# Kernel tuning notes

Measured on AMD Instinct MI355X. Metric: run time of the kernel, lower is better.

## Reference

```python
import jax, jax.numpy as jnp
import numpy as np

N = 50000      # nodes
E = 800000     # edges (avg degree 16)
F0 = 3         # node feature dim
EF = 3         # edge feature dim
C = 4          # num classes


def _lin_params(k, din, dout):
    k1, k2 = jax.random.split(k)
    s = 1.0 / np.sqrt(din)
    W = jax.random.uniform(k1, (dout, din), jnp.float32, -s, s)
    b = jax.random.uniform(k2, (dout,), jnp.float32, -s, s)
    return W, b


def setup_inputs() -> dict:
    key = jax.random.key(0)
    ks = jax.random.split(key, 8)
    x = jax.random.normal(ks[0], (N, F0), jnp.float32)
    edge_index = jax.random.randint(ks[1], (2, E), 0, N, jnp.int32)
    edge_attr = jax.random.uniform(ks[2], (E, EF), dtype=jnp.float32)
    W1, b1 = _lin_params(ks[3], 2 * F0 + EF, 128)
    W2, b2 = _lin_params(ks[4], 2 * 128 + EF, 64)
    W3, b3 = _lin_params(ks[5], 2 * 64 + EF, 32)
    Wc, bc = _lin_params(ks[6], 32, C)
    return dict(x=x, edge_index=edge_index, edge_attr=edge_attr,
                W1=W1, b1=b1, W2=W2, b2=b2, W3=W3, b3=b3, Wc=Wc, bc=bc)


def _edgeconv(x, src, dst, ea, W, b, n):
    # message = Linear(cat([x_i, x_j, edge_attr])); aggregated by scatter-add to dst (x_i side).
    # Split W so the node-side matmuls happen once per node instead of per edge.
    f = x.shape[1]
    Wi, Wj, We = W[:, :f], W[:, f:2 * f], W[:, 2 * f:]
    ai = x @ Wi.T   # [N, out]
    aj = x @ Wj.T   # [N, out]
    msg = ai[dst] + aj[src] + ea @ We.T + b  # [E_aug, out]
    return jax.ops.segment_sum(msg, dst, num_segments=n)


def reference(x, edge_index, edge_attr, W1, b1, W2, b2, W3, b3, Wc, bc):
    n = x.shape[0]
    loops = jnp.arange(n, dtype=edge_index.dtype)
    src = jnp.concatenate([edge_index[0], loops])  # x_j indices
    dst = jnp.concatenate([edge_index[1], loops])  # x_i indices (aggregation targets)
    ea = jnp.concatenate([edge_attr, jnp.zeros((n, edge_attr.shape[1]), edge_attr.dtype)])
    h = jax.nn.relu(_edgeconv(x, src, dst, ea, W1, b1, n))
    h = jax.nn.relu(_edgeconv(h, src, dst, ea, W2, b2, n))
    h = _edgeconv(h, src, dst, ea, W3, b3, n)  # no relu after conv3 in the original
    logits = h @ Wc.T + bc
    return jax.nn.log_softmax(logits, axis=1)
```

## Files before the change

### kernel.cpp

```cpp
#include <hip/hip_runtime.h>
#include <math.h>


static inline size_t align256(size_t x) { return (x + 255) & ~size_t(255); }

typedef unsigned short ushort_t;
using frag8  = __attribute__((ext_vector_type(8))) short;
using f32x4v = __attribute__((ext_vector_type(4))) float;
using half8  = __attribute__((ext_vector_type(8))) _Float16;

__device__ inline unsigned short f2bf(float f) {
    unsigned u = __float_as_uint(f);
    unsigned r = (u + 0x7fffu + ((u >> 16) & 1u)) >> 16;
    return (unsigned short)r;
}
__device__ inline float bflo(unsigned u) { return __uint_as_float(u << 16); }
__device__ inline float bfhi(unsigned u) { return __uint_as_float(u & 0xffff0000u); }


__global__ __launch_bounds__(256) void prep(
    const int* __restrict__ ei, int* __restrict__ count,
    int* __restrict__ pos, int E,
    const float* __restrict__ x, float4* __restrict__ xpad, int n,
    const float* __restrict__ W2, ushort_t* __restrict__ W2bf,
    const float* __restrict__ W3, const float* __restrict__ b3,
    const float* __restrict__ Wc, const float* __restrict__ bc,
    float* __restrict__ AB, float* __restrict__ consts,
    int eb4, int nxb)
{
    const int t = threadIdx.x;
    const int b = blockIdx.x;
    if (b < eb4) {
        int e4 = (b * 256 + t) * 4;
        if (e4 >= E) return;
        if (e4 + 3 < E) {
            int4 d = *(const int4*)(ei + E + e4);
            int4 po;
            po.x = atomicAdd(&count[d.x], 1);
            po.y = atomicAdd(&count[d.y], 1);
            po.z = atomicAdd(&count[d.z], 1);
            po.w = atomicAdd(&count[d.w], 1);
            *(int4*)(pos + e4) = po;
        } else {
            for (int e = e4; e < E; ++e)
                pos[e] = atomicAdd(&count[ei[E + e]], 1);
        }
    } else if (b < eb4 + nxb) {
        int j = (b - eb4) * 256 + t;
        if (j < n) {
            const float* xp = x + (size_t)j * 3;
            xpad[j] = make_float4(xp[0], xp[1], xp[2], 0.f);
        }
    } else if (b < eb4 + nxb + 4) {
        int wb = b - (eb4 + nxb);
        int i0 = wb * 4096 + t;
        int i1 = (wb + 1) * 4096;
        for (int idx = i0; idx < i1; idx += 256) {
            int jg = idx >> 7, k = idx & 127;
            float w = (jg < 64) ? W2[jg * 259 + k] : W2[(jg - 64) * 259 + 128 + k];
            W2bf[idx] = f2bf(w);
        }
    } else {
        for (int idx = t; idx < 512; idx += 256) {
            int j = idx >> 6, k = idx & 63;
            int jj = j & 3;
            int base = (j >= 4) ? 64 : 0;
            float s = 0.f;
            #pragma unroll
            for (int c = 0; c < 32; ++c)
                s += Wc[jj * 32 + c] * W3[c * 131 + base + k];
            AB[idx] = s;
        }
        if (t < 4) {
            float db = 0.f;
            for (int c = 0; c < 32; ++c) db += Wc[t * 32 + c] * b3[c];
            consts[t] = db;
            consts[4 + t] = bc[t];
            for (int q = 0; q < 3; ++q) {
                float s = 0.f;
                for (int c = 0; c < 32; ++c) s += Wc[t * 32 + c] * W3[c * 131 + 128 + q];
                consts[8 + t * 3 + q] = s;
            }
        }
    }
}


__global__ __launch_bounds__(256) void scan_pass1(
    const int* __restrict__ count, int* __restrict__ rowstart,
    int* __restrict__ bsum, int n)
{
    __shared__ int sh[256];
    const int tid = threadIdx.x;
    const int base = blockIdx.x * 1024 + tid * 4;
    int v0 = 0, v1 = 0, v2 = 0, v3 = 0;
    if (base + 3 < n) {
        int4 c = *(const int4*)(count + base);
        v0 = c.x; v1 = c.y; v2 = c.z; v3 = c.w;
    } else {
        if (base + 0 < n) v0 = count[base + 0];
        if (base + 1 < n) v1 = count[base + 1];
        if (base + 2 < n) v2 = count[base + 2];
        if (base + 3 < n) v3 = count[base + 3];
    }
    int tsum = v0 + v1 + v2 + v3;
    sh[tid] = tsum;
    __syncthreads();
    for (int off = 1; off < 256; off <<= 1) {
        int t = (tid >= off) ? sh[tid - off] : 0;
        __syncthreads();
        sh[tid] += t;
        __syncthreads();
    }
    int excl = sh[tid] - tsum;
    int p0 = excl + v0, p1 = p0 + v1, p2 = p1 + v2, p3 = p2 + v3;
    if (base + 0 < n) rowstart[base + 1] = p0;
    if (base + 1 < n) rowstart[base + 2] = p1;
    if (base + 2 < n) rowstart[base + 3] = p2;
    if (base + 3 < n) rowstart[base + 4] = p3;
    if (tid == 255) bsum[blockIdx.x] = sh[255];
}


__global__ __launch_bounds__(256) void csr_scatter2(
    const int* __restrict__ ei, const float* __restrict__ ea,
    const int* __restrict__ pos, const int* __restrict__ rowstart,
    const int* __restrict__ bsum, int nb,
    uint2* __restrict__ csrp, int* __restrict__ rowfin,
    int E, int n, int eb4)
{
    __shared__ int sBex[64];
    const int tid = threadIdx.x;
    if (tid < 64) {
        int v = (tid < nb) ? bsum[tid] : 0;
        int xx = v;
        #pragma unroll
        for (int off = 1; off < 64; off <<= 1) {
            int t = __shfl_up(xx, off);
            if (tid >= off) xx += t;
        }
        sBex[tid] = xx - v;
    }
    __syncthreads();

    if (blockIdx.x < eb4) {
        int e4 = (blockIdx.x * 256 + tid) * 4;
        if (e4 >= E) return;
        if (e4 + 3 < E) {
            int4 s = *(const int4*)(ei + e4);
            int4 d = *(const int4*)(ei + E + e4);
            int4 po = *(const int4*)(pos + e4);
            float4 a = *(const float4*)(ea + (size_t)e4 * 3);
            float4 bq = *(const float4*)(ea + (size_t)e4 * 3 + 4);
            float4 c = *(const float4*)(ea + (size_t)e4 * 3 + 8);
            float ev[12] = { a.x, a.y, a.z, a.w, bq.x, bq.y, bq.z, bq.w, c.x, c.y, c.z, c.w };
            int sv[4] = { s.x, s.y, s.z, s.w };
            int dv[4] = { d.x, d.y, d.z, d.w };
            int pv[4] = { po.x, po.y, po.z, po.w };
            #pragma unroll
            for (int r = 0; r < 4; ++r) {
                uint2 p;
                p.x = (unsigned)f2bf(ev[r * 3 + 0]) | ((unsigned)f2bf(ev[r * 3 + 1]) << 16);
                p.y = (unsigned)f2bf(ev[r * 3 + 2]) | ((unsigned)sv[r] << 16);
                int dd = dv[r];
                int rs = (dd == 0) ? 0 : (rowstart[dd] + sBex[(dd - 1) >> 10]);
                csrp[rs + pv[r]] = p;
            }
        } else {
            for (int e = e4; e < E; ++e) {
                uint2 p;
                p.x = (unsigned)f2bf(ea[e * 3 + 0]) | ((unsigned)f2bf(ea[e * 3 + 1]) << 16);
                p.y = (unsigned)f2bf(ea[e * 3 + 2]) | ((unsigned)ei[e] << 16);
                int dd = ei[E + e];
                int rs = (dd == 0) ? 0 : (rowstart[dd] + sBex[(dd - 1) >> 10]);
                csrp[rs + pos[e]] = p;
            }
        }
    } else {
        int j = (blockIdx.x - eb4) * 256 + tid;
        if (j <= n)
            rowfin[j] = (j == 0) ? 0 : (rowstart[j] + sBex[(j - 1) >> 10]);
    }
}


__global__ __launch_bounds__(256) void h1_gemm(
    const float4* __restrict__ xpad, const float* __restrict__ W1,
    const float* __restrict__ b1, const float* __restrict__ b2,
    const int* __restrict__ rowstart,
    const uint2* __restrict__ csrp, float4* __restrict__ eagg4,
    const ushort_t* __restrict__ W2bf,
    float* __restrict__ AI2, _Float16* __restrict__ AJ2, int n_nodes)
{
    constexpr int HS = 144;
    __shared__ float sM[10 * 128];
    __shared__ ushort_t sH[64 * HS];

    const int tid = threadIdx.x;
    for (int t = tid; t < 1280; t += 256) {
        int k = t >> 7, c = t & 127;
        sM[t] = (k < 9) ? W1[c * 9 + k] : b1[c];
    }
    __syncthreads();

    const int base = blockIdx.x * 64;
    const int wave = tid >> 6, wl = tid & 63;
    const int grp = wl >> 3, ch8 = wl & 7;

    #pragma unroll
    for (int pass = 0; pass < 2; ++pass) {
        int nl = pass * 32 + wave * 8 + grp;
        int n = base + nl;
        float hv[16];
        if (n < n_nodes) {
            int s0 = rowstart[n], s1 = rowstart[n + 1];
            float xx = 0.f, xy = 0.f, xz = 0.f, ex = 0.f, ey = 0.f, ez = 0.f;
            for (int i = s0 + ch8; i < s1; i += 8) {
                uint2 p = csrp[i];
                int s = (int)(p.y >> 16);
                ex += bflo(p.x); ey += bfhi(p.x); ez += bflo(p.y);
                float4 xv = xpad[s];
                xx += xv.x; xy += xv.y; xz += xv.z;
            }
            #pragma unroll
            for (int off = 1; off < 8; off <<= 1) {
                xx += __shfl_xor(xx, off); xy += __shfl_xor(xy, off); xz += __shfl_xor(xz, off);
                ex += __shfl_xor(ex, off); ey += __shfl_xor(ey, off); ez += __shfl_xor(ez, off);
            }
            float deg = (float)(s1 - s0 + 1);
            float4 xs = xpad[n];
            float v[10] = { deg * xs.x, deg * xs.y, deg * xs.z,
                            xs.x + xx, xs.y + xy, xs.z + xz,
                            ex, ey, ez, deg };
            #pragma unroll
            for (int q = 0; q < 16; ++q) {
                int c = ch8 * 16 + q;
                float h = 0.f;
                #pragma unroll
                for (int k = 0; k < 10; ++k) h += v[k] * sM[k * 128 + c];
                hv[q] = fmaxf(h, 0.f);
            }
            if (ch8 == 0) eagg4[n] = make_float4(ex, ey, ez, 0.f);
        } else {
            #pragma unroll
            for (int q = 0; q < 16; ++q) hv[q] = 0.f;
        }
        #pragma unroll
        for (int g = 0; g < 2; ++g) {
            uint4 u;
            u.x = (unsigned)f2bf(hv[g * 8 + 0]) | ((unsigned)f2bf(hv[g * 8 + 1]) << 16);
            u.y = (unsigned)f2bf(hv[g * 8 + 2]) | ((unsigned)f2bf(hv[g * 8 + 3]) << 16);
            u.z = (unsigned)f2bf(hv[g * 8 + 4]) | ((unsigned)f2bf(hv[g * 8 + 5]) << 16);
            u.w = (unsigned)f2bf(hv[g * 8 + 6]) | ((unsigned)f2bf(hv[g * 8 + 7]) << 16);
            *(uint4*)(sH + nl * HS + ch8 * 16 + g * 8) = u;
        }
    }
    __syncthreads();

    const int m = wl & 15, quad = wl >> 4;

    frag8 a[4];
    #pragma unroll
    for (int ks = 0; ks < 4; ++ks)
        a[ks] = *(const frag8*)(sH + (wave * 16 + m) * HS + ks * 32 + quad * 8);

    f32x4v acc[8];
    #pragma unroll
    for (int t = 0; t < 8; ++t) acc[t] = (f32x4v)(0.f);

    #pragma unroll
    for (int t = 0; t < 8; ++t) {
        #pragma unroll
        for (int ks = 0; ks < 4; ++ks) {
            frag8 b = *(const frag8*)(W2bf + (t * 16 + m) * 128 + ks * 32 + quad * 8);
            acc[t] = __builtin_amdgcn_mfma_f32_16x16x32_bf16(a[ks], b, acc[t], 0, 0, 0);
        }
    }

    float b2v[4];
    #pragma unroll
    for (int t = 0; t < 4; ++t) b2v[t] = b2[t * 16 + m];

    #pragma unroll
    for (int reg = 0; reg < 4; ++reg) {
        int grow = base + wave * 16 + quad * 4 + reg;
        if (grow >= n_nodes) continue;
        #pragma unroll
        for (int t = 0; t < 4; ++t)
            AI2[(size_t)grow * 64 + t * 16 + m] = acc[t][reg] + b2v[t];
        #pragma unroll
        for (int t = 4; t < 8; ++t)
            AJ2[(size_t)grow * 64 + (t - 4) * 16 + m] = (_Float16)acc[t][reg];
    }
}


__global__ __launch_bounds__(256) void gather2(
    const float* __restrict__ AI2, const _Float16* __restrict__ AJ2,
    const float* __restrict__ W2,
    const float4* __restrict__ eagg4, const int* __restrict__ rowstart,
    const uint2* __restrict__ csrp, const float* __restrict__ AB,
    float* __restrict__ U, float* __restrict__ Z, int n_nodes)
{
    __shared__ float sAB[512];
    __shared__ float sWe[192];
    const int tid = threadIdx.x;
    for (int t = tid; t < 512; t += 256) sAB[t] = AB[t];
    for (int t = tid; t < 192; t += 256) {
        int c = t / 3, q = t % 3;
        sWe[t] = W2[c * 259 + 256 + q];
    }
    __syncthreads();

    int wl = tid & 63;
    int grp = wl >> 3, ch8 = wl & 7;
    int n = blockIdx.x * 32 + (tid >> 6) * 8 + grp;
    if (n >= n_nodes) return;

    int s0 = rowstart[n], s1 = rowstart[n + 1];

    half8 hacc0 = (half8)(_Float16)0.f;
    half8 hacc1 = (half8)(_Float16)0.f;
    for (int base = s0; base < s1; base += 8) {
        int j = base + ch8;
        if (j >= s1) j = s1 - 1;
        int myidx = (int)(csrp[j].y >> 16);
        int cnt = s1 - base; if (cnt > 8) cnt = 8;
        #pragma unroll
        for (int k = 0; k < 8; ++k) {
            int s = __shfl(myidx, grp * 8 + k);
            if (k < cnt) {
                half8 v = *(const half8*)(AJ2 + (size_t)s * 64 + ch8 * 8);
                if (k & 1) hacc1 += v; else hacc0 += v;
            }
        }
    }
    float acc[8];
    #pragma unroll
    for (int q = 0; q < 8; ++q) acc[q] = (float)hacc0[q] + (float)hacc1[q];

    float deg = (float)(s1 - s0 + 1);
    float4 e4 = eagg4[n];
    const float* aip = AI2 + (size_t)n * 64 + ch8 * 8;
    float4 aiA = *(const float4*)(aip);
    float4 aiB = *(const float4*)(aip + 4);
    half8 su = *(const half8*)(AJ2 + (size_t)n * 64 + ch8 * 8);
    float av[8] = { aiA.x, aiA.y, aiA.z, aiA.w, aiB.x, aiB.y, aiB.z, aiB.w };
    float r[8];
    #pragma unroll
    for (int q = 0; q < 8; ++q) {
        int c = ch8 * 8 + q;
        float we = sWe[c * 3] * e4.x + sWe[c * 3 + 1] * e4.y + sWe[c * 3 + 2] * e4.z;
        r[q] = fmaxf(deg * av[q] + (float)su[q] + we + acc[q], 0.f);
    }
    float pj[8];
    #pragma unroll
    for (int j = 0; j < 8; ++j) {
        float4 wA = *(const float4*)(sAB + j * 64 + ch8 * 8);
        float4 wB = *(const float4*)(sAB + j * 64 + ch8 * 8 + 4);
        pj[j] = r[0] * wA.x + r[1] * wA.y + r[2] * wA.z + r[3] * wA.w
              + r[4] * wB.x + r[5] * wB.y + r[6] * wB.z + r[7] * wB.w;
    }
    #pragma unroll
    for (int off = 1; off < 8; off <<= 1)
        #pragma unroll
        for (int j = 0; j < 8; ++j) pj[j] += __shfl_xor(pj[j], off);

    if (ch8 == 0) {
        *(float4*)(U + (size_t)n * 4) = make_float4(pj[0], pj[1], pj[2], pj[3]);
        *(float4*)(Z + (size_t)n * 4) = make_float4(pj[4], pj[5], pj[6], pj[7]);
    }
}


__global__ __launch_bounds__(256) void final_softmax(
    const float* __restrict__ U, const float* __restrict__ Z,
    const float4* __restrict__ eagg4, const int* __restrict__ rowstart,
    const uint2* __restrict__ csrp, const float* __restrict__ consts,
    float* __restrict__ out, int n_nodes)
{
    int wl = threadIdx.x & 63;
    int grp = wl >> 3, ch8 = wl & 7;
    int n = blockIdx.x * 32 + (threadIdx.x >> 6) * 8 + grp;
    if (n >= n_nodes) return;

    int s0 = rowstart[n], s1 = rowstart[n + 1];
    float ax = 0.f, ay = 0.f, az = 0.f, aw = 0.f;
    for (int i = s0 + ch8; i < s1; i += 8) {
        int s = (int)(csrp[i].y >> 16);
        float4 z = *(const float4*)(Z + (size_t)s * 4);
        ax += z.x; ay += z.y; az += z.z; aw += z.w;
    }
    #pragma unroll
    for (int off = 1; off < 8; off <<= 1) {
        ax += __shfl_xor(ax, off); ay += __shfl_xor(ay, off);
        az += __shfl_xor(az, off); aw += __shfl_xor(aw, off);
    }
    if (ch8 != 0) return;

    float deg = (float)(s1 - s0 + 1);
    float4 u = *(const float4*)(U + (size_t)n * 4);
    float4 zs = *(const float4*)(Z + (size_t)n * 4);
    float4 e4 = eagg4[n];
    float av[4] = { ax + zs.x, ay + zs.y, az + zs.z, aw + zs.w };
    float uv[4] = { u.x, u.y, u.z, u.w };
    float lg[4];
    #pragma unroll
    for (int j = 0; j < 4; ++j) {
        lg[j] = deg * (uv[j] + consts[j]) + av[j] + consts[4 + j]
              + consts[8 + j * 3] * e4.x + consts[9 + j * 3] * e4.y
              + consts[10 + j * 3] * e4.z;
    }
    float m = fmaxf(fmaxf(lg[0], lg[1]), fmaxf(lg[2], lg[3]));
    float lse = logf(expf(lg[0] - m) + expf(lg[1] - m) + expf(lg[2] - m) + expf(lg[3] - m));
    *(float4*)(out + (size_t)n * 4) =
        make_float4(lg[0] - m - lse, lg[1] - m - lse, lg[2] - m - lse, lg[3] - m - lse);
}


extern "C" void kernel_launch(void* const* d_in, const int* in_sizes, int n_in,
                              void* d_out, int out_size, void* d_ws, size_t ws_size,
                              hipStream_t stream)
{
    const float* x    = (const float*)d_in[0];
    const int*   ei   = (const int*)  d_in[1];
    const float* ea   = (const float*)d_in[2];
    const float* W1   = (const float*)d_in[3];
    const float* b1   = (const float*)d_in[4];
    const float* W2   = (const float*)d_in[5];
    const float* b2   = (const float*)d_in[6];
    const float* W3   = (const float*)d_in[7];
    const float* b3   = (const float*)d_in[8];
    const float* Wc   = (const float*)d_in[9];
    const float* bc   = (const float*)d_in[10];
    float* out = (float*)d_out;

    const int N = in_sizes[0] / 3;
    const int E = in_sizes[1] / 2;

    char* ws = (char*)d_ws;
    size_t off = 0;
    int*    count    = (int*)(ws + off);            off = align256(off + (size_t)N * 4);
    int*    pos      = (int*)(ws + off);            off = align256(off + (size_t)E * 4);
    int*    rowstart = (int*)(ws + off);            off = align256(off + (size_t)(N + 1) * 4);
    int*    rowfin   = (int*)(ws + off);            off = align256(off + (size_t)(N + 1) * 4);
    uint2*  csrp     = (uint2*)(ws + off);          off = align256(off + (size_t)E * 8);
    int*    bsum     = (int*)(ws + off);            off = align256(off + 256);
    float*  AB       = (float*)(ws + off);          off = align256(off + 512 * 4);
    float*  consts   = (float*)(ws + off);          off = align256(off + 32 * 4);
    ushort_t* W2bf   = (ushort_t*)(ws + off);       off = align256(off + 128 * 128 * 2);
    float4* xpad     = (float4*)(ws + off);         off = align256(off + (size_t)N * 16);
    float4* eagg4    = (float4*)(ws + off);         off = align256(off + (size_t)N * 16);
    float*  AI2      = (float*)(ws + off);          off = align256(off + (size_t)N * 64 * 4);
    _Float16* AJ2    = (_Float16*)(ws + off);       off = align256(off + (size_t)N * 64 * 2);
    float*  Ubuf     = (float*)(ws + off);          off = align256(off + (size_t)N * 16);
    float*  Zbuf     = (float*)(ws + off);          off = align256(off + (size_t)N * 16);
    (void)ws_size;

    hipMemsetAsync(count, 0, (size_t)N * 4, stream);

    const int eb4 = ((E + 3) / 4 + 255) / 256;
    const int nxb = (N + 255) / 256;
    const int nb1 = (N + 1023) / 1024;
    const int nfb = (N + 1 + 255) / 256;

    prep<<<eb4 + nxb + 5, 256, 0, stream>>>(ei, count, pos, E,
                                            x, xpad, N, W2, W2bf,
                                            W3, b3, Wc, bc, AB, consts,
                                            eb4, nxb);

    scan_pass1<<<nb1, 256, 0, stream>>>(count, rowstart, bsum, N);

    csr_scatter2<<<eb4 + nfb, 256, 0, stream>>>(ei, ea, pos, rowstart, bsum, nb1,
                                                csrp, rowfin, E, N, eb4);

    h1_gemm<<<(N + 63) / 64, 256, 0, stream>>>(xpad, W1, b1, b2, rowfin, csrp,
                                               eagg4, W2bf, AI2, AJ2, N);

    const int gb = (N + 31) / 32;
    gather2<<<gb, 256, 0, stream>>>(AI2, AJ2, W2, eagg4, rowfin, csrp, AB, Ubuf, Zbuf, N);

    final_softmax<<<gb, 256, 0, stream>>>(Ubuf, Zbuf, eagg4, rowfin, csrp, consts, out, N);
}
```

Measured before the change: 198.1 us.

## Embed source features in CSR records and split source-index array

The CSR scatter now gathers each edge's source node features and stores them as fp16 alongside the bf16 edge attributes in a 16-byte record. This removes the dependent xpad gather from the layer-1 aggregation loop, which is also unrolled by two. A separate int array of source indices feeds the later gather kernels, giving them a narrower stream. It also swizzles the W1 shared-memory layout and changes the sH padding to avoid bank conflicts. The cost is double the CSR bytes written plus an extra random gather in the scatter kernel, and fp16 rounding of x.

```diff
diff --git a/kernel.cpp b/kernel.cpp
--- a/kernel.cpp
+++ b/kernel.cpp
@@ -16,6 +16,17 @@
 }
 __device__ inline float bflo(unsigned u) { return __uint_as_float(u << 16); }
 __device__ inline float bfhi(unsigned u) { return __uint_as_float(u & 0xffff0000u); }
+__device__ inline unsigned short f2h(float f) {
+    _Float16 h = (_Float16)f;
+    unsigned short u;
+    __builtin_memcpy(&u, &h, 2);
+    return u;
+}
+__device__ inline float h2f(unsigned short u) {
+    _Float16 h;
+    __builtin_memcpy(&h, &u, 2);
+    return (float)h;
+}
 
 
 __global__ __launch_bounds__(256) void prep(
@@ -126,7 +137,9 @@
     const int* __restrict__ ei, const float* __restrict__ ea,
     const int* __restrict__ pos, const int* __restrict__ rowstart,
     const int* __restrict__ bsum, int nb,
-    uint2* __restrict__ csrp, int* __restrict__ rowfin,
+    const float4* __restrict__ xpad,
+    uint4* __restrict__ csrh, int* __restrict__ csrs,
+    int* __restrict__ rowfin,
     int E, int n, int eb4)
 {
     __shared__ int sBex[64];
@@ -153,27 +166,39 @@
             float4 a = *(const float4*)(ea + (size_t)e4 * 3);
             float4 bq = *(const float4*)(ea + (size_t)e4 * 3 + 4);
             float4 c = *(const float4*)(ea + (size_t)e4 * 3 + 8);
+            float4 xv0 = xpad[s.x], xv1 = xpad[s.y], xv2 = xpad[s.z], xv3 = xpad[s.w];
             float ev[12] = { a.x, a.y, a.z, a.w, bq.x, bq.y, bq.z, bq.w, c.x, c.y, c.z, c.w };
+            float4 xv[4] = { xv0, xv1, xv2, xv3 };
             int sv[4] = { s.x, s.y, s.z, s.w };
             int dv[4] = { d.x, d.y, d.z, d.w };
             int pv[4] = { po.x, po.y, po.z, po.w };
             #pragma unroll
             for (int r = 0; r < 4; ++r) {
-                uint2 p;
-                p.x = (unsigned)f2bf(ev[r * 3 + 0]) | ((unsigned)f2bf(ev[r * 3 + 1]) << 16);
-                p.y = (unsigned)f2bf(ev[r * 3 + 2]) | ((unsigned)sv[r] << 16);
+                uint4 h;
+                h.x = (unsigned)f2bf(ev[r * 3 + 0]) | ((unsigned)f2bf(ev[r * 3 + 1]) << 16);
+                h.y = (unsigned)f2bf(ev[r * 3 + 2]) | ((unsigned)f2h(xv[r].x) << 16);
+                h.z = (unsigned)f2h(xv[r].y) | ((unsigned)f2h(xv[r].z) << 16);
+                h.w = (unsigned)sv[r];
                 int dd = dv[r];
                 int rs = (dd == 0) ? 0 : (rowstart[dd] + sBex[(dd - 1) >> 10]);
-                csrp[rs + pv[r]] = p;
+                int slot = rs + pv[r];
+                csrh[slot] = h;
+                csrs[slot] = sv[r];
             }
         } else {
             for (int e = e4; e < E; ++e) {
-                uint2 p;
-                p.x = (unsigned)f2bf(ea[e * 3 + 0]) | ((unsigned)f2bf(ea[e * 3 + 1]) << 16);
-                p.y = (unsigned)f2bf(ea[e * 3 + 2]) | ((unsigned)ei[e] << 16);
+                int sv = ei[e];
+                float4 xv = xpad[sv];
+                uint4 h;
+                h.x = (unsigned)f2bf(ea[e * 3 + 0]) | ((unsigned)f2bf(ea[e * 3 + 1]) << 16);
+                h.y = (unsigned)f2bf(ea[e * 3 + 2]) | ((unsigned)f2h(xv.x) << 16);
+                h.z = (unsigned)f2h(xv.y) | ((unsigned)f2h(xv.z) << 16);
+                h.w = (unsigned)sv;
                 int dd = ei[E + e];
                 int rs = (dd == 0) ? 0 : (rowstart[dd] + sBex[(dd - 1) >> 10]);
-                csrp[rs + pos[e]] = p;
+                int slot = rs + pos[e];
+                csrh[slot] = h;
+                csrs[slot] = sv;
             }
         }
     } else {
@@ -188,18 +213,19 @@
     const float4* __restrict__ xpad, const float* __restrict__ W1,
     const float* __restrict__ b1, const float* __restrict__ b2,
     const int* __restrict__ rowstart,
-    const uint2* __restrict__ csrp, float4* __restrict__ eagg4,
+    const uint4* __restrict__ csrh, float4* __restrict__ eagg4,
     const ushort_t* __restrict__ W2bf,
     float* __restrict__ AI2, _Float16* __restrict__ AJ2, int n_nodes)
 {
-    constexpr int HS = 144;
+    constexpr int HS = 152;
     __shared__ float sM[10 * 128];
     __shared__ ushort_t sH[64 * HS];
 
     const int tid = threadIdx.x;
     for (int t = tid; t < 1280; t += 256) {
         int k = t >> 7, c = t & 127;
-        sM[t] = (k < 9) ? W1[c * 9 + k] : b1[c];
+        int cp = (c & 15) * 8 + (c >> 4);
+        sM[k * 128 + cp] = (k < 9) ? W1[c * 9 + k] : b1[c];
     }
     __syncthreads();
 
@@ -215,12 +241,25 @@
         if (n < n_nodes) {
             int s0 = rowstart[n], s1 = rowstart[n + 1];
             float xx = 0.f, xy = 0.f, xz = 0.f, ex = 0.f, ey = 0.f, ez = 0.f;
-            for (int i = s0 + ch8; i < s1; i += 8) {
-                uint2 p = csrp[i];
-                int s = (int)(p.y >> 16);
-                ex += bflo(p.x); ey += bfhi(p.x); ez += bflo(p.y);
-                float4 xv = xpad[s];
-                xx += xv.x; xy += xv.y; xz += xv.z;
+            int i = s0 + ch8;
+            for (; i + 8 < s1; i += 16) {
+                uint4 p0 = csrh[i];
+                uint4 p1 = csrh[i + 8];
+                ex += bflo(p0.x); ey += bfhi(p0.x); ez += bflo(p0.y);
+                xx += h2f((ushort_t)(p0.y >> 16));
+                xy += h2f((ushort_t)(p0.z & 0xffff));
+                xz += h2f((ushort_t)(p0.z >> 16));
+                ex += bflo(p1.x); ey += bfhi(p1.x); ez += bflo(p1.y);
+                xx += h2f((ushort_t)(p1.y >> 16));
+                xy += h2f((ushort_t)(p1.z & 0xffff));
+                xz += h2f((ushort_t)(p1.z >> 16));
+            }
+            if (i < s1) {
+                uint4 p0 = csrh[i];
+                ex += bflo(p0.x); ey += bfhi(p0.x); ez += bflo(p0.y);
+                xx += h2f((ushort_t)(p0.y >> 16));
+                xy += h2f((ushort_t)(p0.z & 0xffff));
+                xz += h2f((ushort_t)(p0.z >> 16));
             }
             #pragma unroll
             for (int off = 1; off < 8; off <<= 1) {
@@ -234,10 +273,9 @@
                             ex, ey, ez, deg };
             #pragma unroll
             for (int q = 0; q < 16; ++q) {
-                int c = ch8 * 16 + q;
                 float h = 0.f;
                 #pragma unroll
-                for (int k = 0; k < 10; ++k) h += v[k] * sM[k * 128 + c];
+                for (int k = 0; k < 10; ++k) h += v[k] * sM[k * 128 + q * 8 + ch8];
                 hv[q] = fmaxf(h, 0.f);
             }
             if (ch8 == 0) eagg4[n] = make_float4(ex, ey, ez, 0.f);
@@ -299,7 +337,7 @@
     const float* __restrict__ AI2, const _Float16* __restrict__ AJ2,
     const float* __restrict__ W2,
     const float4* __restrict__ eagg4, const int* __restrict__ rowstart,
-    const uint2* __restrict__ csrp, const float* __restrict__ AB,
+    const int* __restrict__ csrs, const float* __restrict__ AB,
     float* __restrict__ U, float* __restrict__ Z, int n_nodes)
 {
     __shared__ float sAB[512];
@@ -324,7 +362,7 @@
     for (int base = s0; base < s1; base += 8) {
         int j = base + ch8;
         if (j >= s1) j = s1 - 1;
-        int myidx = (int)(csrp[j].y >> 16);
+        int myidx = csrs[j];
         int cnt = s1 - base; if (cnt > 8) cnt = 8;
         #pragma unroll
         for (int k = 0; k < 8; ++k) {
@@ -376,7 +414,7 @@
 __global__ __launch_bounds__(256) void final_softmax(
     const float* __restrict__ U, const float* __restrict__ Z,
     const float4* __restrict__ eagg4, const int* __restrict__ rowstart,
-    const uint2* __restrict__ csrp, const float* __restrict__ consts,
+    const int* __restrict__ csrs, const float* __restrict__ consts,
     float* __restrict__ out, int n_nodes)
 {
     int wl = threadIdx.x & 63;
@@ -387,7 +425,7 @@
     int s0 = rowstart[n], s1 = rowstart[n + 1];
     float ax = 0.f, ay = 0.f, az = 0.f, aw = 0.f;
     for (int i = s0 + ch8; i < s1; i += 8) {
-        int s = (int)(csrp[i].y >> 16);
+        int s = csrs[i];
         float4 z = *(const float4*)(Z + (size_t)s * 4);
         ax += z.x; ay += z.y; az += z.z; aw += z.w;
     }
@@ -444,7 +482,8 @@
     int*    pos      = (int*)(ws + off);            off = align256(off + (size_t)E * 4);
     int*    rowstart = (int*)(ws + off);            off = align256(off + (size_t)(N + 1) * 4);
     int*    rowfin   = (int*)(ws + off);            off = align256(off + (size_t)(N + 1) * 4);
-    uint2*  csrp     = (uint2*)(ws + off);          off = align256(off + (size_t)E * 8);
+    uint4*  csrh     = (uint4*)(ws + off);          off = align256(off + (size_t)E * 16);
+    int*    csrs     = (int*)(ws + off);            off = align256(off + (size_t)E * 4);
     int*    bsum     = (int*)(ws + off);            off = align256(off + 256);
     float*  AB       = (float*)(ws + off);          off = align256(off + 512 * 4);
     float*  consts   = (float*)(ws + off);          off = align256(off + 32 * 4);
@@ -472,13 +511,13 @@
     scan_pass1<<<nb1, 256, 0, stream>>>(count, rowstart, bsum, N);
 
     csr_scatter2<<<eb4 + nfb, 256, 0, stream>>>(ei, ea, pos, rowstart, bsum, nb1,
-                                                csrp, rowfin, E, N, eb4);
-
-    h1_gemm<<<(N + 63) / 64, 256, 0, stream>>>(xpad, W1, b1, b2, rowfin, csrp,
+                                                xpad, csrh, csrs, rowfin, E, N, eb4);
+
+    h1_gemm<<<(N + 63) / 64, 256, 0, stream>>>(xpad, W1, b1, b2, rowfin, csrh,
                                                eagg4, W2bf, AI2, AJ2, N);
 
     const int gb = (N + 31) / 32;
-    gather2<<<gb, 256, 0, stream>>>(AI2, AJ2, W2, eagg4, rowfin, csrp, AB, Ubuf, Zbuf, N);
-
-    final_softmax<<<gb, 256, 0, stream>>>(Ubuf, Zbuf, eagg4, rowfin, csrp, consts, out, N);
-}
+    gather2<<<gb, 256, 0, stream>>>(AI2, AJ2, W2, eagg4, rowfin, csrs, AB, Ubuf, Zbuf, N);
+
+    final_softmax<<<gb, 256, 0, stream>>>(Ubuf, Zbuf, eagg4, rowfin, csrs, consts, out, N);
+}
```

New measurement: 207.1 us. 4.6% more time.

## Aggregate layer-1 neighbor and edge sums via atomics in prep, shrink CSR to indices

Applied to the files above, without the earlier changes.

The layer-1 sums of neighbor features and edge attributes are now accumulated per destination node with float atomics inside the edge-counting prep kernel. This removes h1_gemm's dependency on the CSR build, so h1_gemm can run before the CSR scatter and no longer walks CSR rows. The CSR payload drops from 8-byte packed (bf16 edge attr + src) to 4-byte src index, cutting scatter and gather traffic. The cost is six float atomics per edge, which adds atomic contention and makes the summation order nondeterministic. It also changes the h1 weight layout in shared memory.

```diff
diff --git a/kernel.cpp b/kernel.cpp
--- a/kernel.cpp
+++ b/kernel.cpp
@@ -14,13 +14,12 @@
     unsigned r = (u + 0x7fffu + ((u >> 16) & 1u)) >> 16;
     return (unsigned short)r;
 }
-__device__ inline float bflo(unsigned u) { return __uint_as_float(u << 16); }
-__device__ inline float bfhi(unsigned u) { return __uint_as_float(u & 0xffff0000u); }
 
 
 __global__ __launch_bounds__(256) void prep(
     const int* __restrict__ ei, int* __restrict__ count,
-    int* __restrict__ pos, int E,
+    int* __restrict__ pos, float* __restrict__ nodeacc,
+    const float* __restrict__ ea, int E,
     const float* __restrict__ x, float4* __restrict__ xpad, int n,
     const float* __restrict__ W2, ushort_t* __restrict__ W2bf,
     const float* __restrict__ W3, const float* __restrict__ b3,
@@ -34,6 +33,7 @@
         int e4 = (b * 256 + t) * 4;
         if (e4 >= E) return;
         if (e4 + 3 < E) {
+            int4 s = *(const int4*)(ei + e4);
             int4 d = *(const int4*)(ei + E + e4);
             int4 po;
             po.x = atomicAdd(&count[d.x], 1);
@@ -41,9 +41,37 @@
             po.z = atomicAdd(&count[d.z], 1);
             po.w = atomicAdd(&count[d.w], 1);
             *(int4*)(pos + e4) = po;
+            float4 a = *(const float4*)(ea + (size_t)e4 * 3);
+            float4 bq = *(const float4*)(ea + (size_t)e4 * 3 + 4);
+            float4 c = *(const float4*)(ea + (size_t)e4 * 3 + 8);
+            float ev[12] = { a.x, a.y, a.z, a.w, bq.x, bq.y, bq.z, bq.w, c.x, c.y, c.z, c.w };
+            int sv[4] = { s.x, s.y, s.z, s.w };
+            int dv[4] = { d.x, d.y, d.z, d.w };
+            #pragma unroll
+            for (int r = 0; r < 4; ++r) {
+                const float* xs = x + (size_t)sv[r] * 3;
+                float x0 = xs[0], x1 = xs[1], x2 = xs[2];
+                float* acc = nodeacc + (size_t)dv[r] * 8;
+                atomicAdd(acc + 0, ev[r * 3 + 0]);
+                atomicAdd(acc + 1, ev[r * 3 + 1]);
+                atomicAdd(acc + 2, ev[r * 3 + 2]);
+                atomicAdd(acc + 3, x0);
+                atomicAdd(acc + 4, x1);
+                atomicAdd(acc + 5, x2);
+            }
         } else {
-            for (int e = e4; e < E; ++e)
-                pos[e] = atomicAdd(&count[ei[E + e]], 1);
+            for (int e = e4; e < E; ++e) {
+                int sv = ei[e], dv = ei[E + e];
+                pos[e] = atomicAdd(&count[dv], 1);
+                const float* xs = x + (size_t)sv * 3;
+                float* acc = nodeacc + (size_t)dv * 8;
+                atomicAdd(acc + 0, ea[e * 3 + 0]);
+                atomicAdd(acc + 1, ea[e * 3 + 1]);
+                atomicAdd(acc + 2, ea[e * 3 + 2]);
+                atomicAdd(acc + 3, xs[0]);
+                atomicAdd(acc + 4, xs[1]);
+                atomicAdd(acc + 5, xs[2]);
+            }
         }
     } else if (b < eb4 + nxb) {
         int j = (b - eb4) * 256 + t;
@@ -122,11 +150,108 @@
 }
 
 
+__global__ __launch_bounds__(256) void h1_gemm(
+    const float4* __restrict__ xpad, const float* __restrict__ W1,
+    const float* __restrict__ b1, const float* __restrict__ b2,
+    const int* __restrict__ count, const float* __restrict__ nodeacc,
+    const ushort_t* __restrict__ W2bf,
+    float* __restrict__ AI2, _Float16* __restrict__ AJ2, int n_nodes)
+{
+    constexpr int HS = 152;
+    __shared__ float sM[10 * 128];
+    __shared__ ushort_t sH[64 * HS];
+
+    const int tid = threadIdx.x;
+    for (int t = tid; t < 1280; t += 256) {
+        int k = t >> 7, c = t & 127;
+        int cp = (c & 15) * 8 + (c >> 4);
+        sM[k * 128 + cp] = (k < 9) ? W1[c * 9 + k] : b1[c];
+    }
+    __syncthreads();
+
+    const int base = blockIdx.x * 64;
+    const int wave = tid >> 6, wl = tid & 63;
+    const int grp = wl >> 3, ch8 = wl & 7;
+
+    #pragma unroll
+    for (int pass = 0; pass < 2; ++pass) {
+        int nl = pass * 32 + wave * 8 + grp;
+        int n = base + nl;
+        float hv[16];
+        if (n < n_nodes) {
+            float4 a0 = *(const float4*)(nodeacc + (size_t)n * 8);
+            float4 a1 = *(const float4*)(nodeacc + (size_t)n * 8 + 4);
+            float deg = (float)(count[n] + 1);
+            float4 xs = xpad[n];
+            float v[10] = { deg * xs.x, deg * xs.y, deg * xs.z,
+                            xs.x + a0.w, xs.y + a1.x, xs.z + a1.y,
+                            a0.x, a0.y, a0.z, deg };
+            #pragma unroll
+            for (int q = 0; q < 16; ++q) {
+                float h = 0.f;
+                #pragma unroll
+                for (int k = 0; k < 10; ++k) h += v[k] * sM[k * 128 + q * 8 + ch8];
+                hv[q] = fmaxf(h, 0.f);
+            }
+        } else {
+            #pragma unroll
+            for (int q = 0; q < 16; ++q) hv[q] = 0.f;
+        }
+        #pragma unroll
+        for (int g = 0; g < 2; ++g) {
+            uint4 u;
+            u.x = (unsigned)f2bf(hv[g * 8 + 0]) | ((unsigned)f2bf(hv[g * 8 + 1]) << 16);
+            u.y = (unsigned)f2bf(hv[g * 8 + 2]) | ((unsigned)f2bf(hv[g * 8 + 3]) << 16);
+            u.z = (unsigned)f2bf(hv[g * 8 + 4]) | ((unsigned)f2bf(hv[g * 8 + 5]) << 16);
+            u.w = (unsigned)f2bf(hv[g * 8 + 6]) | ((unsigned)f2bf(hv[g * 8 + 7]) << 16);
+            *(uint4*)(sH + nl * HS + ch8 * 16 + g * 8) = u;
+        }
+    }
+    __syncthreads();
+
+    const int m = wl & 15, quad = wl >> 4;
+
+    frag8 a[4];
+    #pragma unroll
+    for (int ks = 0; ks < 4; ++ks)
+        a[ks] = *(const frag8*)(sH + (wave * 16 + m) * HS + ks * 32 + quad * 8);
+
+    f32x4v acc[8];
+    #pragma unroll
+    for (int t = 0; t < 8; ++t) acc[t] = (f32x4v)(0.f);
+
+    #pragma unroll
+    for (int t = 0; t < 8; ++t) {
+        #pragma unroll
+        for (int ks = 0; ks < 4; ++ks) {
+            frag8 b = *(const frag8*)(W2bf + (t * 16 + m) * 128 + ks * 32 + quad * 8);
+            acc[t] = __builtin_amdgcn_mfma_f32_16x16x32_bf16(a[ks], b, acc[t], 0, 0, 0);
+        }
+    }
+
+    float b2v[4];
+    #pragma unroll
+    for (int t = 0; t < 4; ++t) b2v[t] = b2[t * 16 + m];
+
+    #pragma unroll
+    for (int reg = 0; reg < 4; ++reg) {
+        int grow = base + wave * 16 + quad * 4 + reg;
+        if (grow >= n_nodes) continue;
+        #pragma unroll
+        for (int t = 0; t < 4; ++t)
+            AI2[(size_t)grow * 64 + t * 16 + m] = acc[t][reg] + b2v[t];
+        #pragma unroll
+        for (int t = 4; t < 8; ++t)
+            AJ2[(size_t)grow * 64 + (t - 4) * 16 + m] = (_Float16)acc[t][reg];
+    }
+}
+
+
 __global__ __launch_bounds__(256) void csr_scatter2(
-    const int* __restrict__ ei, const float* __restrict__ ea,
+    const int* __restrict__ ei,
     const int* __restrict__ pos, const int* __restrict__ rowstart,
     const int* __restrict__ bsum, int nb,
-    uint2* __restrict__ csrp, int* __restrict__ rowfin,
+    int* __restrict__ csrs, int* __restrict__ rowfin,
     int E, int n, int eb4)
 {
     __shared__ int sBex[64];
@@ -150,30 +275,20 @@
             int4 s = *(const int4*)(ei + e4);
             int4 d = *(const int4*)(ei + E + e4);
             int4 po = *(const int4*)(pos + e4);
-            float4 a = *(const float4*)(ea + (size_t)e4 * 3);
-            float4 bq = *(const float4*)(ea + (size_t)e4 * 3 + 4);
-            float4 c = *(const float4*)(ea + (size_t)e4 * 3 + 8);
-            float ev[12] = { a.x, a.y, a.z, a.w, bq.x, bq.y, bq.z, bq.w, c.x, c.y, c.z, c.w };
             int sv[4] = { s.x, s.y, s.z, s.w };
             int dv[4] = { d.x, d.y, d.z, d.w };
             int pv[4] = { po.x, po.y, po.z, po.w };
             #pragma unroll
             for (int r = 0; r < 4; ++r) {
-                uint2 p;
-                p.x = (unsigned)f2bf(ev[r * 3 + 0]) | ((unsigned)f2bf(ev[r * 3 + 1]) << 16);
-                p.y = (unsigned)f2bf(ev[r * 3 + 2]) | ((unsigned)sv[r] << 16);
                 int dd = dv[r];
                 int rs = (dd == 0) ? 0 : (rowstart[dd] + sBex[(dd - 1) >> 10]);
-                csrp[rs + pv[r]] = p;
+                csrs[rs + pv[r]] = sv[r];
             }
         } else {
             for (int e = e4; e < E; ++e) {
-                uint2 p;
-                p.x = (unsigned)f2bf(ea[e * 3 + 0]) | ((unsigned)f2bf(ea[e * 3 + 1]) << 16);
-                p.y = (unsigned)f2bf(ea[e * 3 + 2]) | ((unsigned)ei[e] << 16);
                 int dd = ei[E + e];
                 int rs = (dd == 0) ? 0 : (rowstart[dd] + sBex[(dd - 1) >> 10]);
-                csrp[rs + pos[e]] = p;
+                csrs[rs + pos[e]] = ei[e];
             }
         }
     } else {
@@ -184,122 +299,11 @@
 }
 
 
-__global__ __launch_bounds__(256) void h1_gemm(
-    const float4* __restrict__ xpad, const float* __restrict__ W1,
-    const float* __restrict__ b1, const float* __restrict__ b2,
-    const int* __restrict__ rowstart,
-    const uint2* __restrict__ csrp, float4* __restrict__ eagg4,
-    const ushort_t* __restrict__ W2bf,
-    float* __restrict__ AI2, _Float16* __restrict__ AJ2, int n_nodes)
-{
-    constexpr int HS = 144;
-    __shared__ float sM[10 * 128];
-    __shared__ ushort_t sH[64 * HS];
-
-    const int tid = threadIdx.x;
-    for (int t = tid; t < 1280; t += 256) {
-        int k = t >> 7, c = t & 127;
-        sM[t] = (k < 9) ? W1[c * 9 + k] : b1[c];
-    }
-    __syncthreads();
-
-    const int base = blockIdx.x * 64;
-    const int wave = tid >> 6, wl = tid & 63;
-    const int grp = wl >> 3, ch8 = wl & 7;
-
-    #pragma unroll
-    for (int pass = 0; pass < 2; ++pass) {
-        int nl = pass * 32 + wave * 8 + grp;
-        int n = base + nl;
-        float hv[16];
-        if (n < n_nodes) {
-            int s0 = rowstart[n], s1 = rowstart[n + 1];
-            float xx = 0.f, xy = 0.f, xz = 0.f, ex = 0.f, ey = 0.f, ez = 0.f;
-            for (int i = s0 + ch8; i < s1; i += 8) {
-                uint2 p = csrp[i];
-                int s = (int)(p.y >> 16);
-                ex += bflo(p.x); ey += bfhi(p.x); ez += bflo(p.y);
-                float4 xv = xpad[s];
-                xx += xv.x; xy += xv.y; xz += xv.z;
-            }
-            #pragma unroll
-            for (int off = 1; off < 8; off <<= 1) {
-                xx += __shfl_xor(xx, off); xy += __shfl_xor(xy, off); xz += __shfl_xor(xz, off);
-                ex += __shfl_xor(ex, off); ey += __shfl_xor(ey, off); ez += __shfl_xor(ez, off);
-            }
-            float deg = (float)(s1 - s0 + 1);
-            float4 xs = xpad[n];
-            float v[10] = { deg * xs.x, deg * xs.y, deg * xs.z,
-                            xs.x + xx, xs.y + xy, xs.z + xz,
-                            ex, ey, ez, deg };
-            #pragma unroll
-            for (int q = 0; q < 16; ++q) {
-                int c = ch8 * 16 + q;
-                float h = 0.f;
-                #pragma unroll
-                for (int k = 0; k < 10; ++k) h += v[k] * sM[k * 128 + c];
-                hv[q] = fmaxf(h, 0.f);
-            }
-            if (ch8 == 0) eagg4[n] = make_float4(ex, ey, ez, 0.f);
-        } else {
-            #pragma unroll
-            for (int q = 0; q < 16; ++q) hv[q] = 0.f;
-        }
-        #pragma unroll
-        for (int g = 0; g < 2; ++g) {
-            uint4 u;
-            u.x = (unsigned)f2bf(hv[g * 8 + 0]) | ((unsigned)f2bf(hv[g * 8 + 1]) << 16);
-            u.y = (unsigned)f2bf(hv[g * 8 + 2]) | ((unsigned)f2bf(hv[g * 8 + 3]) << 16);
-            u.z = (unsigned)f2bf(hv[g * 8 + 4]) | ((unsigned)f2bf(hv[g * 8 + 5]) << 16);
-            u.w = (unsigned)f2bf(hv[g * 8 + 6]) | ((unsigned)f2bf(hv[g * 8 + 7]) << 16);
-            *(uint4*)(sH + nl * HS + ch8 * 16 + g * 8) = u;
-        }
-    }
-    __syncthreads();
-
-    const int m = wl & 15, quad = wl >> 4;
-
-    frag8 a[4];
-    #pragma unroll
-    for (int ks = 0; ks < 4; ++ks)
-        a[ks] = *(const frag8*)(sH + (wave * 16 + m) * HS + ks * 32 + quad * 8);
-
-    f32x4v acc[8];
-    #pragma unroll
-    for (int t = 0; t < 8; ++t) acc[t] = (f32x4v)(0.f);
-
-    #pragma unroll
-    for (int t = 0; t < 8; ++t) {
-        #pragma unroll
-        for (int ks = 0; ks < 4; ++ks) {
-            frag8 b = *(const frag8*)(W2bf + (t * 16 + m) * 128 + ks * 32 + quad * 8);
-            acc[t] = __builtin_amdgcn_mfma_f32_16x16x32_bf16(a[ks], b, acc[t], 0, 0, 0);
-        }
-    }
-
-    float b2v[4];
-    #pragma unroll
-    for (int t = 0; t < 4; ++t) b2v[t] = b2[t * 16 + m];
-
-    #pragma unroll
-    for (int reg = 0; reg < 4; ++reg) {
-        int grow = base + wave * 16 + quad * 4 + reg;
-        if (grow >= n_nodes) continue;
-        #pragma unroll
-        for (int t = 0; t < 4; ++t)
-            AI2[(size_t)grow * 64 + t * 16 + m] = acc[t][reg] + b2v[t];
-        #pragma unroll
-        for (int t = 4; t < 8; ++t)
-            AJ2[(size_t)grow * 64 + (t - 4) * 16 + m] = (_Float16)acc[t][reg];
-    }
-}
-
-
 __global__ __launch_bounds__(256) void gather2(
     const float* __restrict__ AI2, const _Float16* __restrict__ AJ2,
-    const float* __restrict__ W2,
-    const float4* __restrict__ eagg4, const int* __restrict__ rowstart,
-    const uint2* __restrict__ csrp, const float* __restrict__ AB,
+    const float* __restrict__ W2, const float* __restrict__ nodeacc,
+    const int* __restrict__ rowstart,
+    const int* __restrict__ csrs, const float* __restrict__ AB,
     float* __restrict__ U, float* __restrict__ Z, int n_nodes)
 {
     __shared__ float sAB[512];
@@ -324,7 +328,7 @@
     for (int base = s0; base < s1; base += 8) {
         int j = base + ch8;
         if (j >= s1) j = s1 - 1;
-        int myidx = (int)(csrp[j].y >> 16);
+        int myidx = csrs[j];
         int cnt = s1 - base; if (cnt > 8) cnt = 8;
         #pragma unroll
         for (int k = 0; k < 8; ++k) {
@@ -340,7 +344,7 @@
     for (int q = 0; q < 8; ++q) acc[q] = (float)hacc0[q] + (float)hacc1[q];
 
     float deg = (float)(s1 - s0 + 1);
-    float4 e4 = eagg4[n];
+    float4 e4 = *(const float4*)(nodeacc + (size_t)n * 8);
     const float* aip = AI2 + (size_t)n * 64 + ch8 * 8;
     float4 aiA = *(const float4*)(aip);
     float4 aiB = *(const float4*)(aip + 4);
@@ -375,8 +379,8 @@
 
 __global__ __launch_bounds__(256) void final_softmax(
     const float* __restrict__ U, const float* __restrict__ Z,
-    const float4* __restrict__ eagg4, const int* __restrict__ rowstart,
-    const uint2* __restrict__ csrp, const float* __restrict__ consts,
+    const float* __restrict__ nodeacc, const int* __restrict__ rowstart,
+    const int* __restrict__ csrs, const float* __restrict__ consts,
     float* __restrict__ out, int n_nodes)
 {
     int wl = threadIdx.x & 63;
@@ -387,7 +391,7 @@
     int s0 = rowstart[n], s1 = rowstart[n + 1];
     float ax = 0.f, ay = 0.f, az = 0.f, aw = 0.f;
     for (int i = s0 + ch8; i < s1; i += 8) {
-        int s = (int)(csrp[i].y >> 16);
+        int s = csrs[i];
         float4 z = *(const float4*)(Z + (size_t)s * 4);
         ax += z.x; ay += z.y; az += z.z; aw += z.w;
     }
@@ -401,7 +405,7 @@
     float deg = (float)(s1 - s0 + 1);
     float4 u = *(const float4*)(U + (size_t)n * 4);
     float4 zs = *(const float4*)(Z + (size_t)n * 4);
-    float4 e4 = eagg4[n];
+    float4 e4 = *(const float4*)(nodeacc + (size_t)n * 8);
     float av[4] = { ax + zs.x, ay + zs.y, az + zs.z, aw + zs.w };
     float uv[4] = { u.x, u.y, u.z, u.w };
     float lg[4];
@@ -441,44 +445,45 @@
     char* ws = (char*)d_ws;
     size_t off = 0;
     int*    count    = (int*)(ws + off);            off = align256(off + (size_t)N * 4);
+    float*  nodeacc  = (float*)(ws + off);          off = align256(off + (size_t)N * 32);
     int*    pos      = (int*)(ws + off);            off = align256(off + (size_t)E * 4);
     int*    rowstart = (int*)(ws + off);            off = align256(off + (size_t)(N + 1) * 4);
     int*    rowfin   = (int*)(ws + off);            off = align256(off + (size_t)(N + 1) * 4);
-    uint2*  csrp     = (uint2*)(ws + off);          off = align256(off + (size_t)E * 8);
+    int*    csrs     = (int*)(ws + off);            off = align256(off + (size_t)E * 4);
     int*    bsum     = (int*)(ws + off);            off = align256(off + 256);
     float*  AB       = (float*)(ws + off);          off = align256(off + 512 * 4);
     float*  consts   = (float*)(ws + off);          off = align256(off + 32 * 4);
     ushort_t* W2bf   = (ushort_t*)(ws + off);       off = align256(off + 128 * 128 * 2);
     float4* xpad     = (float4*)(ws + off);         off = align256(off + (size_t)N * 16);
-    float4* eagg4    = (float4*)(ws + off);         off = align256(off + (size_t)N * 16);
     float*  AI2      = (float*)(ws + off);          off = align256(off + (size_t)N * 64 * 4);
     _Float16* AJ2    = (_Float16*)(ws + off);       off = align256(off + (size_t)N * 64 * 2);
     float*  Ubuf     = (float*)(ws + off);          off = align256(off + (size_t)N * 16);
     float*  Zbuf     = (float*)(ws + off);          off = align256(off + (size_t)N * 16);
     (void)ws_size;
 
-    hipMemsetAsync(count, 0, (size_t)N * 4, stream);
+    size_t zlen = (size_t)((char*)nodeacc - (char*)count) + (size_t)N * 32;
+    hipMemsetAsync(count, 0, zlen, stream);
 
     const int eb4 = ((E + 3) / 4 + 255) / 256;
     const int nxb = (N + 255) / 256;
     const int nb1 = (N + 1023) / 1024;
     const int nfb = (N + 1 + 255) / 256;
 
-    prep<<<eb4 + nxb + 5, 256, 0, stream>>>(ei, count, pos, E,
+    prep<<<eb4 + nxb + 5, 256, 0, stream>>>(ei, count, pos, nodeacc, ea, E,
                                             x, xpad, N, W2, W2bf,
                                             W3, b3, Wc, bc, AB, consts,
                                             eb4, nxb);
 
     scan_pass1<<<nb1, 256, 0, stream>>>(count, rowstart, bsum, N);
 
-    csr_scatter2<<<eb4 + nfb, 256, 0, stream>>>(ei, ea, pos, rowstart, bsum, nb1,
-                                                csrp, rowfin, E, N, eb4);
-
-    h1_gemm<<<(N + 63) / 64, 256, 0, stream>>>(xpad, W1, b1, b2, rowfin, csrp,
-                                               eagg4, W2bf, AI2, AJ2, N);
+    h1_gemm<<<(N + 63) / 64, 256, 0, stream>>>(xpad, W1, b1, b2, count, nodeacc,
+                                               W2bf, AI2, AJ2, N);
+
+    csr_scatter2<<<eb4 + nfb, 256, 0, stream>>>(ei, pos, rowstart, bsum, nb1,
+                                                csrs, rowfin, E, N, eb4);
 
     const int gb = (N + 31) / 32;
-    gather2<<<gb, 256, 0, stream>>>(AI2, AJ2, W2, eagg4, rowfin, csrp, AB, Ubuf, Zbuf, N);
-
-    final_softmax<<<gb, 256, 0, stream>>>(Ubuf, Zbuf, eagg4, rowfin, csrp, consts, out, N);
-}
+    gather2<<<gb, 256, 0, stream>>>(AI2, AJ2, W2, nodeacc, rowfin, csrs, AB, Ubuf, Zbuf, N);
+
+    final_softmax<<<gb, 256, 0, stream>>>(Ubuf, Zbuf, nodeacc, rowfin, csrs, consts, out, N);
+}
```

New measurement: 430.5 us. 2.17x slower.

## Aggregate layer-1 neighbor sums per block with shared-memory atomics over edge range

Applied to the files above, without the earlier changes.

Replaces the per-node 8-lane CSR gather loop in h1_gemm with a block-wide sweep over the block's contiguous edge range. Each thread binary-searches the owning node and accumulates into shared memory with atomics. This aims to spread load evenly across threads instead of idling lanes on low-degree nodes. It also transposes the W1 shared layout to avoid bank conflicts and pads the sH stride. The cost is many LDS atomics per edge plus a 6-step search per edge.

```diff
diff --git a/kernel.cpp b/kernel.cpp
--- a/kernel.cpp
+++ b/kernel.cpp
@@ -187,23 +187,55 @@
 __global__ __launch_bounds__(256) void h1_gemm(
     const float4* __restrict__ xpad, const float* __restrict__ W1,
     const float* __restrict__ b1, const float* __restrict__ b2,
-    const int* __restrict__ rowstart,
+    const int* __restrict__ rowfin,
     const uint2* __restrict__ csrp, float4* __restrict__ eagg4,
     const ushort_t* __restrict__ W2bf,
     float* __restrict__ AI2, _Float16* __restrict__ AJ2, int n_nodes)
 {
-    constexpr int HS = 144;
+    constexpr int HS = 152;
     __shared__ float sM[10 * 128];
+    __shared__ float sAcc[64 * 8];
+    __shared__ int   sRE[65];
     __shared__ ushort_t sH[64 * HS];
 
     const int tid = threadIdx.x;
+    const int base = blockIdx.x * 64;
+
     for (int t = tid; t < 1280; t += 256) {
         int k = t >> 7, c = t & 127;
-        sM[t] = (k < 9) ? W1[c * 9 + k] : b1[c];
-    }
+        int cp = (c & 15) * 8 + (c >> 4);
+        sM[k * 128 + cp] = (k < 9) ? W1[c * 9 + k] : b1[c];
+    }
+    if (tid < 65) {
+        int j = base + tid;
+        sRE[tid] = rowfin[j < n_nodes ? j : n_nodes];
+    }
+    sAcc[tid] = 0.f;
+    sAcc[tid + 256] = 0.f;
     __syncthreads();
 
-    const int base = blockIdx.x * 64;
+    {
+        const int s0 = sRE[0], s1 = sRE[64];
+        for (int i = s0 + tid; i < s1; i += 256) {
+            uint2 p = csrp[i];
+            float4 xv = xpad[(int)(p.y >> 16)];
+            int lo = 0;
+            #pragma unroll
+            for (int step = 32; step >= 1; step >>= 1) {
+                int mid = lo + step;
+                if (i >= sRE[mid]) lo = mid;
+            }
+            float* a = sAcc + lo * 8;
+            atomicAdd(a + 0, bflo(p.x));
+            atomicAdd(a + 1, bfhi(p.x));
+            atomicAdd(a + 2, bflo(p.y));
+            atomicAdd(a + 3, xv.x);
+            atomicAdd(a + 4, xv.y);
+            atomicAdd(a + 5, xv.z);
+        }
+    }
+    __syncthreads();
+
     const int wave = tid >> 6, wl = tid & 63;
     const int grp = wl >> 3, ch8 = wl & 7;
 
@@ -213,31 +245,18 @@
         int n = base + nl;
         float hv[16];
         if (n < n_nodes) {
-            int s0 = rowstart[n], s1 = rowstart[n + 1];
-            float xx = 0.f, xy = 0.f, xz = 0.f, ex = 0.f, ey = 0.f, ez = 0.f;
-            for (int i = s0 + ch8; i < s1; i += 8) {
-                uint2 p = csrp[i];
-                int s = (int)(p.y >> 16);
-                ex += bflo(p.x); ey += bfhi(p.x); ez += bflo(p.y);
-                float4 xv = xpad[s];
-                xx += xv.x; xy += xv.y; xz += xv.z;
-            }
-            #pragma unroll
-            for (int off = 1; off < 8; off <<= 1) {
-                xx += __shfl_xor(xx, off); xy += __shfl_xor(xy, off); xz += __shfl_xor(xz, off);
-                ex += __shfl_xor(ex, off); ey += __shfl_xor(ey, off); ez += __shfl_xor(ez, off);
-            }
-            float deg = (float)(s1 - s0 + 1);
+            float ex = sAcc[nl * 8 + 0], ey = sAcc[nl * 8 + 1], ez = sAcc[nl * 8 + 2];
+            float xx = sAcc[nl * 8 + 3], xy = sAcc[nl * 8 + 4], xz = sAcc[nl * 8 + 5];
+            float deg = (float)(sRE[nl + 1] - sRE[nl] + 1);
             float4 xs = xpad[n];
             float v[10] = { deg * xs.x, deg * xs.y, deg * xs.z,
                             xs.x + xx, xs.y + xy, xs.z + xz,
                             ex, ey, ez, deg };
             #pragma unroll
             for (int q = 0; q < 16; ++q) {
-                int c = ch8 * 16 + q;
                 float h = 0.f;
                 #pragma unroll
-                for (int k = 0; k < 10; ++k) h += v[k] * sM[k * 128 + c];
+                for (int k = 0; k < 10; ++k) h += v[k] * sM[k * 128 + q * 8 + ch8];
                 hv[q] = fmaxf(h, 0.f);
             }
             if (ch8 == 0) eagg4[n] = make_float4(ex, ey, ez, 0.f);
```

Result: slower. 230.3 us (+16.3%).
